# Performance work log

Measured on AMD Instinct MI355X. Metric: run time of the kernel, lower is better.

Reference implementation:

```python
import jax, jax.numpy as jnp
import numpy as np

N_NODES = 50000
N_GRAPHS = 250
NODES_PER_GRAPH = 200
EDGES_PER_GRAPH = 3200  # avg degree 16
F_IN = 128
EMB = 128
HID = 128
VOCAB = 1000
N_REL = 8


def setup_inputs() -> dict:
    key = jax.random.key(0)
    ks = jax.random.split(key, 16)

    # message: col 0 = discrete token id (stored as float), col 1 = continuous value
    disc = jax.random.randint(ks[0], (N_GRAPHS,), 0, VOCAB).astype(jnp.float32)
    cont = jax.random.normal(ks[1], (N_GRAPHS,), dtype=jnp.float32)
    message = jnp.stack([disc, cont], axis=1)  # [B, 2]

    x = jax.random.normal(ks[2], (N_NODES, F_IN), dtype=jnp.float32)

    # within-graph edges: local indices + per-graph node offset
    offs = (jnp.arange(N_GRAPHS, dtype=jnp.int64) * NODES_PER_GRAPH)[:, None]
    src = (jax.random.randint(ks[3], (N_GRAPHS, EDGES_PER_GRAPH), 0, NODES_PER_GRAPH) + offs).reshape(-1)
    dst = (jax.random.randint(ks[4], (N_GRAPHS, EDGES_PER_GRAPH), 0, NODES_PER_GRAPH) + offs).reshape(-1)
    edge_index = jnp.stack([src, dst], axis=0).astype(jnp.int64)  # [2, E]
    edge_type = jax.random.randint(ks[5], (N_GRAPHS * EDGES_PER_GRAPH,), 0, N_REL).astype(jnp.int64)

    batch = jnp.repeat(jnp.arange(N_GRAPHS, dtype=jnp.int64), NODES_PER_GRAPH)  # [N]

    s = 0.05
    W1 = jax.random.normal(ks[6], (N_REL, F_IN, EMB), dtype=jnp.float32) * s
    root1 = jax.random.normal(ks[7], (F_IN, EMB), dtype=jnp.float32) * s
    b1 = jnp.zeros((EMB,), dtype=jnp.float32)
    W2 = jax.random.normal(ks[8], (N_REL, EMB, EMB), dtype=jnp.float32) * s
    root2 = jax.random.normal(ks[9], (EMB, EMB), dtype=jnp.float32) * s
    b2 = jnp.zeros((EMB,), dtype=jnp.float32)
    embed_table = jax.random.normal(ks[10], (VOCAB, EMB), dtype=jnp.float32) * s
    cont_w = jax.random.normal(ks[11], (1, EMB), dtype=jnp.float32) * s
    cont_b = jnp.zeros((EMB,), dtype=jnp.float32)
    msg_w = jax.random.normal(ks[12], (2 * EMB, HID), dtype=jnp.float32) * s
    msg_b = jnp.zeros((HID,), dtype=jnp.float32)

    return {
        "message": message, "x": x, "edge_index": edge_index, "edge_type": edge_type,
        "batch": batch, "max_nodes": NODES_PER_GRAPH,
        "W1": W1, "root1": root1, "b1": b1, "W2": W2, "root2": root2, "b2": b2,
        "embed_table": embed_table, "cont_w": cont_w, "cont_b": cont_b,
        "msg_w": msg_w, "msg_b": msg_b,
    }


def _rgcn_conv(h, src, dst, edge_type, W, root, b, n_nodes, n_rel):
    # per-node per-relation transform, then gather per edge: avoids [E,F,F] weight gather
    hW = jnp.einsum('nf,rfo->nro', h, W)          # [N, R, O]
    msg = hW[src, edge_type]                       # [E, O]
    # mean aggregation per (dst, relation) as in PyG RGCNConv(aggr='mean')
    key_dr = dst * n_rel + edge_type
    cnt = jax.ops.segment_sum(jnp.ones_like(edge_type, dtype=h.dtype), key_dr,
                              num_segments=n_nodes * n_rel)
    norm = 1.0 / jnp.maximum(cnt[key_dr], 1.0)     # [E]
    agg = jax.ops.segment_sum(msg * norm[:, None], dst, num_segments=n_nodes)  # [N, O]
    return agg + h @ root + b


def reference(message, x, edge_index, edge_type, batch, max_nodes,
              W1, root1, b1, W2, root2, b2,
              embed_table, cont_w, cont_b, msg_w, msg_b):
    n_nodes = x.shape[0]
    n_rel = W1.shape[0]
    n_graphs = message.shape[0]
    src, dst = edge_index[0], edge_index[1]

    # --- RGCN node embeddings (2 layers, ReLU between) ---
    h = _rgcn_conv(x, src, dst, edge_type, W1, root1, b1, n_nodes, n_rel)
    h = jax.nn.relu(h)
    node_emb = _rgcn_conv(h, src, dst, edge_type, W2, root2, b2, n_nodes, n_rel)  # [N, EMB]

    # --- message representation ---
    disc_tok = message[:, 0].astype(jnp.int32)
    disc_emb = embed_table[disc_tok]                                   # [B, EMB]
    cont_emb = jax.nn.relu(message[:, 1:2] @ cont_w + cont_b)          # [B, EMB]
    combined = jnp.concatenate([disc_emb, cont_emb], axis=1)           # [B, 2*EMB]
    message_repr = jax.nn.relu(combined @ msg_w + msg_b)               # [B, HID]

    # --- per-node dot score against its graph's message, padded per graph ---
    scores = jnp.einsum('ne,ne->n', node_emb, message_repr[batch])     # [N]
    counts = jax.ops.segment_sum(jnp.ones((n_nodes,), dtype=jnp.int32), batch,
                                 num_segments=n_graphs)
    start = jnp.cumsum(counts) - counts                                # exclusive cumsum
    pos = jnp.arange(n_nodes) - start[batch]                           # slot within graph
    logits = jnp.full((n_graphs, max_nodes), -jnp.inf, dtype=scores.dtype)
    logits = logits.at[batch, pos].set(scores)
    return logits
```

## Files before the change

kernel.cpp:

```cpp
#include <hip/hip_runtime.h>
#include <stdint.h>

#define G_   250
#define P_   200
#define EPG  3200
#define E_   800000
#define F_   128
#define R_   8
#define HROW 136
#define NKEY (R_ * P_)
#define BSTG (8 * 4 * 64 * 8)

typedef _Float16 f16x8 __attribute__((ext_vector_type(8)));
typedef _Float16 f16x4 __attribute__((ext_vector_type(4)));
typedef float    f32x4 __attribute__((ext_vector_type(4)));
typedef float    f32x16 __attribute__((ext_vector_type(16)));

__global__ __launch_bounds__(256) void k_wstage(const float* __restrict__ W1, const float* __restrict__ root1,
                                                const float* __restrict__ W2, const float* __restrict__ root2,
                                                _Float16* __restrict__ wf) {
  int t = blockIdx.x * 256 + threadIdx.x;
  int j    = t & 7;
  int lane = (t >> 3) & 63;
  int ntj  = (t >> 9) & 3;
  int kt   = (t >> 11) & 7;
  int rl_  = t >> 14;
  int r = rl_ % 9, l = rl_ / 9;
  const float* Wl = (l == 0) ? W1 : W2;
  const float* rt = (l == 0) ? root1 : root2;
  int k = kt * 16 + (lane >> 5) * 8 + j;
  int n = ntj * 32 + (lane & 31);
  float v = (r < 8) ? Wl[(r * F_ + k) * F_ + n] : rt[k * F_ + n];
  wf[t] = (_Float16)v;
}

__global__ __launch_bounds__(512, 1) void k_main(
    const float* __restrict__ x, const int* __restrict__ ei, const int* __restrict__ et,
    const _Float16* __restrict__ wf, const float* __restrict__ b1, const float* __restrict__ b2,
    const float* __restrict__ message, const float* __restrict__ embed,
    const float* __restrict__ cw, const float* __restrict__ cb,
    const float* __restrict__ mw, const float* __restrict__ mb,
    float* __restrict__ out) {
  __shared__ __attribute__((aligned(16))) _Float16 hbuf0[P_ * HROW];
  __shared__ __attribute__((aligned(16))) _Float16 hbuf1[P_ * HROW];
  __shared__ __attribute__((aligned(16))) _Float16 Bstage[BSTG];
  __shared__ unsigned short csrS[EPG];
  __shared__ int offsS[NKEY + 1];
  __shared__ float msgS[F_ + 1];

  int g = blockIdx.x, tid = threadIdx.x;
  int lane = tid & 63, wave = tid >> 6;
  int m32 = lane & 31, kh = lane >> 5;

  int*   Sint = (int*)hbuf1;
  int*   cnt  = Sint;
  int*   cur  = Sint + 1600;
  int*   eRec = Sint + 3200;
  float* comb = (float*)(Sint + 6400);
  float* red  = (float*)(Sint + 6656);

  f16x8 st0[4];
#pragma unroll
  for (int i = 0; i < 4; i++)
    st0[i] = *((const f16x8*)(wf + i * 4096 + tid * 8));

  for (int i = tid; i < P_ * 32; i += 512) {
    int row = i >> 5, c4 = i & 31;
    const float4 v = ((const float4*)x)[(g * P_ + row) * 32 + c4];
    f16x4 pk = { (_Float16)v.x, (_Float16)v.y, (_Float16)v.z, (_Float16)v.w };
    *((f16x4*)&hbuf0[row * HROW + c4 * 4]) = pk;
  }
  for (int i = tid; i < NKEY; i += 512) { cnt[i] = 0; cur[i] = 0; }
  if (tid < F_) {
    int tok = (int)message[g * 2];
    float cont = message[g * 2 + 1];
    comb[tid] = embed[tok * F_ + tid];
    float ce = cont * cw[tid] + cb[tid];
    comb[F_ + tid] = ce > 0.0f ? ce : 0.0f;
  }
#pragma unroll
  for (int i = 0; i < 4; i++)
    *((f16x8*)(Bstage + i * 4096 + tid * 8)) = st0[i];
  __syncthreads();

  int base = g * EPG, nbase = g * P_;
  if (wave < 6) {
    for (int e = wave * 64 + lane; e < EPG; e += 384) {
      int s = ei[base + e] - nbase;
      int d = ei[E_ + base + e] - nbase;
      int r = et[base + e];
      eRec[e] = s | (d << 8) | (r << 16);
      atomicAdd(&cnt[r * P_ + d], 1);
    }
  } else {
    int col = tid & 127;
    float acc = 0.0f;
#pragma unroll 16
    for (int k2 = 0; k2 < 256; k2++) acc += comb[k2] * mw[k2 * F_ + col];
    red[col] = acc;
  }
  __syncthreads();

  if (wave == 0) {
    int4 vv[8];
    int osum = 0;
    if (lane < 50) {
      const int4* cp = (const int4*)(cnt + lane * 32);
#pragma unroll
      for (int i = 0; i < 8; i++) { vv[i] = cp[i]; osum += vv[i].x + vv[i].y + vv[i].z + vv[i].w; }
    }
    int incl = osum;
#pragma unroll
    for (int d = 1; d < 64; d <<= 1) {
      int t2 = __shfl_up(incl, d, 64);
      if (lane >= d) incl += t2;
    }
    int run = incl - osum;
    if (lane < 50) {
#pragma unroll
      for (int i = 0; i < 8; i++) {
        offsS[lane * 32 + i * 4 + 0] = run; run += vv[i].x;
        offsS[lane * 32 + i * 4 + 1] = run; run += vv[i].y;
        offsS[lane * 32 + i * 4 + 2] = run; run += vv[i].z;
        offsS[lane * 32 + i * 4 + 3] = run; run += vv[i].w;
      }
    }
    if (lane == 0) offsS[NKEY] = EPG;
  } else if (wave == 1) {
    float m0 = mb[lane] + red[lane];
    float m1 = mb[lane + 64] + red[lane + 64];
    m0 = m0 > 0.0f ? m0 : 0.0f;
    m1 = m1 > 0.0f ? m1 : 0.0f;
    msgS[lane] = m0; msgS[lane + 64] = m1;
    float p = m0 * b2[lane] + m1 * b2[lane + 64];
#pragma unroll
    for (int d = 32; d > 0; d >>= 1) p += __shfl_xor(p, d, 64);
    if (lane == 0) msgS[F_] = p;
  }
  __syncthreads();

  for (int e = tid; e < EPG; e += 512) {
    int rec = eRec[e];
    int s = rec & 255, d = (rec >> 8) & 255, r = rec >> 16;
    int key = r * P_ + d;
    int pos = atomicAdd(&cur[key], 1);
    csrS[offsS[key] + pos] = (unsigned short)s;
  }
  __syncthreads();

  int jobBase = wave * 25;
  bool rowAct = (m32 < 25);
  int myD = jobBase + m32;
  int ck = kh * 8;

  for (int l = 0; l < 2; l++) {
    const _Float16* Ap = (l == 0) ? hbuf0 : hbuf1;
    _Float16* balt = (l == 0) ? hbuf1 : hbuf0;
    f32x16 acc[4];
#pragma unroll
    for (int nt = 0; nt < 4; nt++)
#pragma unroll
      for (int i = 0; i < 16; i++) acc[nt][i] = 0.0f;
    const _Float16* wl = wf + l * (9 * BSTG);
    for (int r = 0; r < 9; r++) {
      f16x8 st2[4];
      bool haveNext = (r < 8) || (l == 0);
      if (haveNext) {
        const _Float16* wnext = (r < 8) ? (wl + (r + 1) * BSTG) : (wf + 9 * BSTG);
#pragma unroll
        for (int i = 0; i < 4; i++)
          st2[i] = *((const f16x8*)(wnext + i * 4096 + tid * 8));
      }
      f16x8 a[8];
      if (r < 8) {
        int o = 0, n = 0;
        if (rowAct) { int key = r * P_ + myD; o = offsS[key]; n = offsS[key + 1] - o; }
        f16x8 z = {0, 0, 0, 0, 0, 0, 0, 0};
#pragma unroll
        for (int kt = 0; kt < 8; kt++) a[kt] = z;
        int t = 0;
        for (; t + 2 <= n; t += 2) {
          int s0 = (int)csrS[o + t];
          int s1 = (int)csrS[o + t + 1];
          const _Float16* hp0 = &Ap[s0 * HROW + ck];
          const _Float16* hp1 = &Ap[s1 * HROW + ck];
          f16x8 u0[8], u1[8];
#pragma unroll
          for (int kt = 0; kt < 8; kt++) u0[kt] = *((const f16x8*)(hp0 + kt * 16));
#pragma unroll
          for (int kt = 0; kt < 8; kt++) u1[kt] = *((const f16x8*)(hp1 + kt * 16));
#pragma unroll
          for (int kt = 0; kt < 8; kt++) a[kt] += u0[kt] + u1[kt];
        }
        if (t < n) {
          int s0 = (int)csrS[o + t];
          const _Float16* hp0 = &Ap[s0 * HROW + ck];
#pragma unroll
          for (int kt = 0; kt < 8; kt++) a[kt] += *((const f16x8*)(hp0 + kt * 16));
        }
        float nf = (n > 0) ? 1.0f / (float)n : 0.0f;
        _Float16 nh = (_Float16)nf;
#pragma unroll
        for (int kt = 0; kt < 8; kt++) a[kt] *= nh;
      } else {
        int rowA = jobBase + (rowAct ? m32 : 24);
        const _Float16* hp = &Ap[rowA * HROW + ck];
#pragma unroll
        for (int kt = 0; kt < 8; kt++) a[kt] = *((const f16x8*)(hp + kt * 16));
      }
      const _Float16* bp = (r & 1) ? balt : Bstage;
#pragma unroll
      for (int kt = 0; kt < 8; kt++) {
#pragma unroll
        for (int nt = 0; nt < 4; nt++) {
          f16x8 b = *((const f16x8*)&bp[((kt * 4 + nt) * 64 + lane) * 8]);
          acc[nt] = __builtin_amdgcn_mfma_f32_32x32x16_f16(a[kt], b, acc[nt], 0, 0, 0);
        }
      }
      if (r < 8) {
        _Float16* dst = ((r + 1) & 1) ? balt : Bstage;
#pragma unroll
        for (int i = 0; i < 4; i++)
          *((f16x8*)(dst + i * 4096 + tid * 8)) = st2[i];
        __syncthreads();
      } else if (l == 0) {
        __syncthreads();
#pragma unroll
        for (int i = 0; i < 4; i++)
          *((f16x8*)(Bstage + i * 4096 + tid * 8)) = st2[i];
      }
    }
    if (l == 0) {
#pragma unroll
      for (int nt = 0; nt < 4; nt++) {
        int col = nt * 32 + m32;
        float bias = b1[col];
#pragma unroll
        for (int reg = 0; reg < 16; reg++) {
          int row = (reg & 3) + 8 * (reg >> 2) + 4 * kh;
          if (row < 25) {
            float v = acc[nt][reg] + bias;
            v = v > 0.0f ? v : 0.0f;
            hbuf1[(jobBase + row) * HROW + col] = (_Float16)v;
          }
        }
      }
      __syncthreads();
    } else {
      float db2 = msgS[F_];
#pragma unroll
      for (int reg = 0; reg < 16; reg++) {
        int row = (reg & 3) + 8 * (reg >> 2) + 4 * kh;
        float p = 0.0f;
#pragma unroll
        for (int nt = 0; nt < 4; nt++)
          p += acc[nt][reg] * msgS[nt * 32 + m32];
        p += __shfl_xor(p, 16, 32);
        p += __shfl_xor(p, 8, 32);
        p += __shfl_xor(p, 4, 32);
        p += __shfl_xor(p, 2, 32);
        p += __shfl_xor(p, 1, 32);
        if (m32 == 0 && row < 25)
          out[g * P_ + jobBase + row] = p + db2;
      }
    }
  }
}

extern "C" void kernel_launch(void* const* d_in, const int* in_sizes, int n_in,
                              void* d_out, int out_size, void* d_ws, size_t ws_size,
                              hipStream_t stream) {
  const float* message = (const float*)d_in[0];
  const float* x       = (const float*)d_in[1];
  const int*   ei      = (const int*)d_in[2];
  const int*   et      = (const int*)d_in[3];
  const float* W1      = (const float*)d_in[6];
  const float* root1   = (const float*)d_in[7];
  const float* b1      = (const float*)d_in[8];
  const float* W2      = (const float*)d_in[9];
  const float* root2   = (const float*)d_in[10];
  const float* b2      = (const float*)d_in[11];
  const float* embed   = (const float*)d_in[12];
  const float* cw      = (const float*)d_in[13];
  const float* cb      = (const float*)d_in[14];
  const float* mw      = (const float*)d_in[15];
  const float* mb      = (const float*)d_in[16];

  _Float16* wfrag = (_Float16*)d_ws;
  float*    out   = (float*)d_out;

  hipLaunchKernelGGL(k_wstage, dim3(1152), dim3(256), 0, stream, W1, root1, W2, root2, wfrag);
  hipLaunchKernelGGL(k_main, dim3(G_), dim3(512), 0, stream, x, ei, et, wfrag, b1, b2,
                     message, embed, cw, cb, mw, mb, out);
}
```

Before: 172.3 us.

## Double block size to 1024 threads, splitting output columns across wave pairs

Raises the main kernel from 512 to 1024 threads per graph. Each pair of waves shares a 25-row job and splits the 128 output columns in half, and the final dot-product partials are combined through shared memory. The goal is more latency hiding in the gather and MFMA phases. The cost is that each wave now repeats the full neighbour gather for its rows, doubling LDS gather traffic. The unrolled two-edge gather loop is also simplified back to one edge per iteration. The launch bound of (1024, 4) may force register limits.

```diff
diff --git a/kernel.cpp b/kernel.cpp
--- a/kernel.cpp
+++ b/kernel.cpp
@@ -34,7 +34,7 @@
   wf[t] = (_Float16)v;
 }
 
-__global__ __launch_bounds__(512, 1) void k_main(
+__global__ __launch_bounds__(1024, 4) void k_main(
     const float* __restrict__ x, const int* __restrict__ ei, const int* __restrict__ et,
     const _Float16* __restrict__ wf, const float* __restrict__ b1, const float* __restrict__ b2,
     const float* __restrict__ message, const float* __restrict__ embed,
@@ -47,6 +47,7 @@
   __shared__ unsigned short csrS[EPG];
   __shared__ int offsS[NKEY + 1];
   __shared__ float msgS[F_ + 1];
+  __shared__ float scoreS[2 * P_];
 
   int g = blockIdx.x, tid = threadIdx.x;
   int lane = tid & 63, wave = tid >> 6;
@@ -59,18 +60,17 @@
   float* comb = (float*)(Sint + 6400);
   float* red  = (float*)(Sint + 6656);
 
-  f16x8 st0[4];
-#pragma unroll
-  for (int i = 0; i < 4; i++)
-    st0[i] = *((const f16x8*)(wf + i * 4096 + tid * 8));
-
-  for (int i = tid; i < P_ * 32; i += 512) {
+  f16x8 st0[2];
+  st0[0] = *((const f16x8*)(wf + tid * 8));
+  st0[1] = *((const f16x8*)(wf + 8192 + tid * 8));
+
+  for (int i = tid; i < P_ * 32; i += 1024) {
     int row = i >> 5, c4 = i & 31;
     const float4 v = ((const float4*)x)[(g * P_ + row) * 32 + c4];
     f16x4 pk = { (_Float16)v.x, (_Float16)v.y, (_Float16)v.z, (_Float16)v.w };
     *((f16x4*)&hbuf0[row * HROW + c4 * 4]) = pk;
   }
-  for (int i = tid; i < NKEY; i += 512) { cnt[i] = 0; cur[i] = 0; }
+  for (int i = tid; i < NKEY; i += 1024) { cnt[i] = 0; cur[i] = 0; }
   if (tid < F_) {
     int tok = (int)message[g * 2];
     float cont = message[g * 2 + 1];
@@ -78,26 +78,26 @@
     float ce = cont * cw[tid] + cb[tid];
     comb[F_ + tid] = ce > 0.0f ? ce : 0.0f;
   }
-#pragma unroll
-  for (int i = 0; i < 4; i++)
-    *((f16x8*)(Bstage + i * 4096 + tid * 8)) = st0[i];
+  *((f16x8*)(Bstage + tid * 8)) = st0[0];
+  *((f16x8*)(Bstage + 8192 + tid * 8)) = st0[1];
   __syncthreads();
 
   int base = g * EPG, nbase = g * P_;
-  if (wave < 6) {
-    for (int e = wave * 64 + lane; e < EPG; e += 384) {
+  if (wave == 12 || wave == 13) {
+    int col = tid & 127;
+    float acc = 0.0f;
+#pragma unroll 16
+    for (int k2 = 0; k2 < 256; k2++) acc += comb[k2] * mw[k2 * F_ + col];
+    red[col] = acc;
+  } else {
+    int iw = (wave < 12) ? wave : (wave - 2);
+    for (int e = iw * 64 + lane; e < EPG; e += 896) {
       int s = ei[base + e] - nbase;
       int d = ei[E_ + base + e] - nbase;
       int r = et[base + e];
       eRec[e] = s | (d << 8) | (r << 16);
       atomicAdd(&cnt[r * P_ + d], 1);
     }
-  } else {
-    int col = tid & 127;
-    float acc = 0.0f;
-#pragma unroll 16
-    for (int k2 = 0; k2 < 256; k2++) acc += comb[k2] * mw[k2 * F_ + col];
-    red[col] = acc;
   }
   __syncthreads();
 
@@ -139,7 +139,7 @@
   }
   __syncthreads();
 
-  for (int e = tid; e < EPG; e += 512) {
+  for (int e = tid; e < EPG; e += 1024) {
     int rec = eRec[e];
     int s = rec & 255, d = (rec >> 8) & 255, r = rec >> 16;
     int key = r * P_ + d;
@@ -148,28 +148,29 @@
   }
   __syncthreads();
 
-  int jobBase = wave * 25;
+  int rh = wave >> 1, ch = wave & 1;
+  int jobBase = rh * 25;
   bool rowAct = (m32 < 25);
   int myD = jobBase + m32;
   int ck = kh * 8;
+  int ntB = ch * 2;
 
   for (int l = 0; l < 2; l++) {
     const _Float16* Ap = (l == 0) ? hbuf0 : hbuf1;
     _Float16* balt = (l == 0) ? hbuf1 : hbuf0;
-    f32x16 acc[4];
-#pragma unroll
-    for (int nt = 0; nt < 4; nt++)
+    f32x16 acc[2];
+#pragma unroll
+    for (int nt = 0; nt < 2; nt++)
 #pragma unroll
       for (int i = 0; i < 16; i++) acc[nt][i] = 0.0f;
     const _Float16* wl = wf + l * (9 * BSTG);
     for (int r = 0; r < 9; r++) {
-      f16x8 st2[4];
+      f16x8 st2[2];
       bool haveNext = (r < 8) || (l == 0);
       if (haveNext) {
         const _Float16* wnext = (r < 8) ? (wl + (r + 1) * BSTG) : (wf + 9 * BSTG);
-#pragma unroll
-        for (int i = 0; i < 4; i++)
-          st2[i] = *((const f16x8*)(wnext + i * 4096 + tid * 8));
+        st2[0] = *((const f16x8*)(wnext + tid * 8));
+        st2[1] = *((const f16x8*)(wnext + 8192 + tid * 8));
       }
       f16x8 a[8];
       if (r < 8) {
@@ -178,21 +179,7 @@
         f16x8 z = {0, 0, 0, 0, 0, 0, 0, 0};
 #pragma unroll
         for (int kt = 0; kt < 8; kt++) a[kt] = z;
-        int t = 0;
-        for (; t + 2 <= n; t += 2) {
-          int s0 = (int)csrS[o + t];
-          int s1 = (int)csrS[o + t + 1];
-          const _Float16* hp0 = &Ap[s0 * HROW + ck];
-          const _Float16* hp1 = &Ap[s1 * HROW + ck];
-          f16x8 u0[8], u1[8];
-#pragma unroll
-          for (int kt = 0; kt < 8; kt++) u0[kt] = *((const f16x8*)(hp0 + kt * 16));
-#pragma unroll
-          for (int kt = 0; kt < 8; kt++) u1[kt] = *((const f16x8*)(hp1 + kt * 16));
-#pragma unroll
-          for (int kt = 0; kt < 8; kt++) a[kt] += u0[kt] + u1[kt];
-        }
-        if (t < n) {
+        for (int t = 0; t < n; t++) {
           int s0 = (int)csrS[o + t];
           const _Float16* hp0 = &Ap[s0 * HROW + ck];
 #pragma unroll
@@ -212,34 +199,32 @@
 #pragma unroll
       for (int kt = 0; kt < 8; kt++) {
 #pragma unroll
-        for (int nt = 0; nt < 4; nt++) {
-          f16x8 b = *((const f16x8*)&bp[((kt * 4 + nt) * 64 + lane) * 8]);
-          acc[nt] = __builtin_amdgcn_mfma_f32_32x32x16_f16(a[kt], b, acc[nt], 0, 0, 0);
+        for (int ntl = 0; ntl < 2; ntl++) {
+          f16x8 b = *((const f16x8*)&bp[((kt * 4 + ntB + ntl) * 64 + lane) * 8]);
+          acc[ntl] = __builtin_amdgcn_mfma_f32_32x32x16_f16(a[kt], b, acc[ntl], 0, 0, 0);
         }
       }
       if (r < 8) {
         _Float16* dst = ((r + 1) & 1) ? balt : Bstage;
-#pragma unroll
-        for (int i = 0; i < 4; i++)
-          *((f16x8*)(dst + i * 4096 + tid * 8)) = st2[i];
+        *((f16x8*)(dst + tid * 8)) = st2[0];
+        *((f16x8*)(dst + 8192 + tid * 8)) = st2[1];
         __syncthreads();
       } else if (l == 0) {
         __syncthreads();
-#pragma unroll
-        for (int i = 0; i < 4; i++)
-          *((f16x8*)(Bstage + i * 4096 + tid * 8)) = st2[i];
+        *((f16x8*)(Bstage + tid * 8)) = st2[0];
+        *((f16x8*)(Bstage + 8192 + tid * 8)) = st2[1];
       }
     }
     if (l == 0) {
 #pragma unroll
-      for (int nt = 0; nt < 4; nt++) {
-        int col = nt * 32 + m32;
+      for (int ntl = 0; ntl < 2; ntl++) {
+        int col = (ntB + ntl) * 32 + m32;
         float bias = b1[col];
 #pragma unroll
         for (int reg = 0; reg < 16; reg++) {
           int row = (reg & 3) + 8 * (reg >> 2) + 4 * kh;
           if (row < 25) {
-            float v = acc[nt][reg] + bias;
+            float v = acc[ntl][reg] + bias;
             v = v > 0.0f ? v : 0.0f;
             hbuf1[(jobBase + row) * HROW + col] = (_Float16)v;
           }
@@ -247,22 +232,23 @@
       }
       __syncthreads();
     } else {
-      float db2 = msgS[F_];
+      float mg0 = msgS[ntB * 32 + m32];
+      float mg1 = msgS[(ntB + 1) * 32 + m32];
 #pragma unroll
       for (int reg = 0; reg < 16; reg++) {
         int row = (reg & 3) + 8 * (reg >> 2) + 4 * kh;
-        float p = 0.0f;
-#pragma unroll
-        for (int nt = 0; nt < 4; nt++)
-          p += acc[nt][reg] * msgS[nt * 32 + m32];
+        float p = acc[0][reg] * mg0 + acc[1][reg] * mg1;
         p += __shfl_xor(p, 16, 32);
         p += __shfl_xor(p, 8, 32);
         p += __shfl_xor(p, 4, 32);
         p += __shfl_xor(p, 2, 32);
         p += __shfl_xor(p, 1, 32);
         if (m32 == 0 && row < 25)
-          out[g * P_ + jobBase + row] = p + db2;
-      }
+          scoreS[ch * P_ + jobBase + row] = p;
+      }
+      __syncthreads();
+      if (tid < P_)
+        out[g * P_ + tid] = scoreS[tid] + scoreS[P_ + tid] + msgS[F_];
     }
   }
 }
@@ -290,6 +276,6 @@
   float*    out   = (float*)d_out;
 
   hipLaunchKernelGGL(k_wstage, dim3(1152), dim3(256), 0, stream, W1, root1, W2, root2, wfrag);
-  hipLaunchKernelGGL(k_main, dim3(G_), dim3(512), 0, stream, x, ei, et, wfrag, b1, b2,
+  hipLaunchKernelGGL(k_main, dim3(G_), dim3(1024), 0, stream, x, ei, et, wfrag, b1, b2,
                      message, embed, cw, cb, mw, mb, out);
 }
```

New measurement: 184.2 us. 1.07x slower.

## Software-pipeline relation gathers with MFMA using double A-register buffers

Applied to the files above, without the earlier changes.

Restructures the per-relation loop into pairs so the neighbour gather for the next relation is issued right after the MFMA block of the current one, using two A-fragment register sets (aA/aB). MFMA sections are wrapped in s_setprio to favour matrix issue while other waves gather. The goal is to overlap LDS gather latency with matrix compute across waves. It raises register pressure, which could cause spills under the one-block-per-CU 512-thread launch bound.

```diff
diff --git a/kernel.cpp b/kernel.cpp
--- a/kernel.cpp
+++ b/kernel.cpp
@@ -34,6 +34,62 @@
   wf[t] = (_Float16)v;
 }
 
+__device__ __forceinline__ void gather_rel(f16x8 (&a)[8], const _Float16* __restrict__ Ap,
+                                           const unsigned short* __restrict__ csr,
+                                           const int* __restrict__ offs,
+                                           int key, bool rowAct, int ck) {
+  int o = 0, n = 0;
+  if (rowAct) { o = offs[key]; n = offs[key + 1] - o; }
+  f16x8 z = {0, 0, 0, 0, 0, 0, 0, 0};
+#pragma unroll
+  for (int kt = 0; kt < 8; kt++) a[kt] = z;
+  int t = 0;
+  for (; t + 2 <= n; t += 2) {
+    int s0 = (int)csr[o + t];
+    int s1 = (int)csr[o + t + 1];
+    const _Float16* hp0 = &Ap[s0 * HROW + ck];
+    const _Float16* hp1 = &Ap[s1 * HROW + ck];
+    f16x8 u0[8], u1[8];
+#pragma unroll
+    for (int kt = 0; kt < 8; kt++) u0[kt] = *((const f16x8*)(hp0 + kt * 16));
+#pragma unroll
+    for (int kt = 0; kt < 8; kt++) u1[kt] = *((const f16x8*)(hp1 + kt * 16));
+#pragma unroll
+    for (int kt = 0; kt < 8; kt++) a[kt] += u0[kt] + u1[kt];
+  }
+  if (t < n) {
+    int s0 = (int)csr[o + t];
+    const _Float16* hp0 = &Ap[s0 * HROW + ck];
+#pragma unroll
+    for (int kt = 0; kt < 8; kt++) a[kt] += *((const f16x8*)(hp0 + kt * 16));
+  }
+  float nf = (n > 0) ? 1.0f / (float)n : 0.0f;
+  _Float16 nh = (_Float16)nf;
+#pragma unroll
+  for (int kt = 0; kt < 8; kt++) a[kt] *= nh;
+}
+
+__device__ __forceinline__ void gather_root(f16x8 (&a)[8], const _Float16* __restrict__ Ap,
+                                            int rowA, int ck) {
+  const _Float16* hp = &Ap[rowA * HROW + ck];
+#pragma unroll
+  for (int kt = 0; kt < 8; kt++) a[kt] = *((const f16x8*)(hp + kt * 16));
+}
+
+__device__ __forceinline__ void mfma_rel(f32x16 (&acc)[4], const f16x8 (&a)[8],
+                                         const _Float16* __restrict__ bp, int lane) {
+  __builtin_amdgcn_s_setprio(1);
+#pragma unroll
+  for (int kt = 0; kt < 8; kt++) {
+#pragma unroll
+    for (int nt = 0; nt < 4; nt++) {
+      f16x8 b = *((const f16x8*)&bp[((kt * 4 + nt) * 64 + lane) * 8]);
+      acc[nt] = __builtin_amdgcn_mfma_f32_32x32x16_f16(a[kt], b, acc[nt], 0, 0, 0);
+    }
+  }
+  __builtin_amdgcn_s_setprio(0);
+}
+
 __global__ __launch_bounds__(512, 1) void k_main(
     const float* __restrict__ x, const int* __restrict__ ei, const int* __restrict__ et,
     const _Float16* __restrict__ wf, const float* __restrict__ b1, const float* __restrict__ b2,
@@ -152,6 +208,7 @@
   bool rowAct = (m32 < 25);
   int myD = jobBase + m32;
   int ck = kh * 8;
+  int rowA = jobBase + (rowAct ? m32 : 24);
 
   for (int l = 0; l < 2; l++) {
     const _Float16* Ap = (l == 0) ? hbuf0 : hbuf1;
@@ -162,75 +219,52 @@
 #pragma unroll
       for (int i = 0; i < 16; i++) acc[nt][i] = 0.0f;
     const _Float16* wl = wf + l * (9 * BSTG);
-    for (int r = 0; r < 9; r++) {
+
+    f16x8 aA[8], aB[8];
+    gather_rel(aA, Ap, csrS, offsS, 0 * P_ + myD, rowAct, ck);
+
+    for (int p = 0; p < 4; p++) {
+      int r1 = 2 * p + 1;
       f16x8 st2[4];
-      bool haveNext = (r < 8) || (l == 0);
-      if (haveNext) {
-        const _Float16* wnext = (r < 8) ? (wl + (r + 1) * BSTG) : (wf + 9 * BSTG);
+      {
+        const _Float16* wn = wl + r1 * BSTG;
 #pragma unroll
         for (int i = 0; i < 4; i++)
-          st2[i] = *((const f16x8*)(wnext + i * 4096 + tid * 8));
-      }
-      f16x8 a[8];
-      if (r < 8) {
-        int o = 0, n = 0;
-        if (rowAct) { int key = r * P_ + myD; o = offsS[key]; n = offsS[key + 1] - o; }
-        f16x8 z = {0, 0, 0, 0, 0, 0, 0, 0};
-#pragma unroll
-        for (int kt = 0; kt < 8; kt++) a[kt] = z;
-        int t = 0;
-        for (; t + 2 <= n; t += 2) {
-          int s0 = (int)csrS[o + t];
-          int s1 = (int)csrS[o + t + 1];
-          const _Float16* hp0 = &Ap[s0 * HROW + ck];
-          const _Float16* hp1 = &Ap[s1 * HROW + ck];
-          f16x8 u0[8], u1[8];
-#pragma unroll
-          for (int kt = 0; kt < 8; kt++) u0[kt] = *((const f16x8*)(hp0 + kt * 16));
-#pragma unroll
-          for (int kt = 0; kt < 8; kt++) u1[kt] = *((const f16x8*)(hp1 + kt * 16));
-#pragma unroll
-          for (int kt = 0; kt < 8; kt++) a[kt] += u0[kt] + u1[kt];
-        }
-        if (t < n) {
-          int s0 = (int)csrS[o + t];
-          const _Float16* hp0 = &Ap[s0 * HROW + ck];
-#pragma unroll
-          for (int kt = 0; kt < 8; kt++) a[kt] += *((const f16x8*)(hp0 + kt * 16));
-        }
-        float nf = (n > 0) ? 1.0f / (float)n : 0.0f;
-        _Float16 nh = (_Float16)nf;
-#pragma unroll
-        for (int kt = 0; kt < 8; kt++) a[kt] *= nh;
-      } else {
-        int rowA = jobBase + (rowAct ? m32 : 24);
-        const _Float16* hp = &Ap[rowA * HROW + ck];
-#pragma unroll
-        for (int kt = 0; kt < 8; kt++) a[kt] = *((const f16x8*)(hp + kt * 16));
-      }
-      const _Float16* bp = (r & 1) ? balt : Bstage;
-#pragma unroll
-      for (int kt = 0; kt < 8; kt++) {
-#pragma unroll
-        for (int nt = 0; nt < 4; nt++) {
-          f16x8 b = *((const f16x8*)&bp[((kt * 4 + nt) * 64 + lane) * 8]);
-          acc[nt] = __builtin_amdgcn_mfma_f32_32x32x16_f16(a[kt], b, acc[nt], 0, 0, 0);
-        }
-      }
-      if (r < 8) {
-        _Float16* dst = ((r + 1) & 1) ? balt : Bstage;
+          st2[i] = *((const f16x8*)(wn + i * 4096 + tid * 8));
+      }
+      mfma_rel(acc, aA, Bstage, lane);
+      gather_rel(aB, Ap, csrS, offsS, r1 * P_ + myD, rowAct, ck);
+#pragma unroll
+      for (int i = 0; i < 4; i++)
+        *((f16x8*)(balt + i * 4096 + tid * 8)) = st2[i];
+      __syncthreads();
+      {
+        const _Float16* wn = wl + (r1 + 1) * BSTG;
 #pragma unroll
         for (int i = 0; i < 4; i++)
-          *((f16x8*)(dst + i * 4096 + tid * 8)) = st2[i];
-        __syncthreads();
-      } else if (l == 0) {
-        __syncthreads();
-#pragma unroll
-        for (int i = 0; i < 4; i++)
-          *((f16x8*)(Bstage + i * 4096 + tid * 8)) = st2[i];
-      }
+          st2[i] = *((const f16x8*)(wn + i * 4096 + tid * 8));
+      }
+      mfma_rel(acc, aB, balt, lane);
+      if (p < 3)
+        gather_rel(aA, Ap, csrS, offsS, (2 * p + 2) * P_ + myD, rowAct, ck);
+      else
+        gather_root(aA, Ap, rowA, ck);
+#pragma unroll
+      for (int i = 0; i < 4; i++)
+        *((f16x8*)(Bstage + i * 4096 + tid * 8)) = st2[i];
+      __syncthreads();
     }
     if (l == 0) {
+      f16x8 st3[4];
+      const _Float16* wn = wf + 9 * BSTG;
+#pragma unroll
+      for (int i = 0; i < 4; i++)
+        st3[i] = *((const f16x8*)(wn + i * 4096 + tid * 8));
+      mfma_rel(acc, aA, Bstage, lane);
+      __syncthreads();
+#pragma unroll
+      for (int i = 0; i < 4; i++)
+        *((f16x8*)(Bstage + i * 4096 + tid * 8)) = st3[i];
 #pragma unroll
       for (int nt = 0; nt < 4; nt++) {
         int col = nt * 32 + m32;
@@ -247,6 +281,7 @@
       }
       __syncthreads();
     } else {
+      mfma_rel(acc, aA, Bstage, lane);
       float db2 = msgS[F_];
 #pragma unroll
       for (int reg = 0; reg < 16; reg++) {
```

Result: no change. 169.2 us (-1.8%).
